# Performance work log

Measured on AMD Instinct MI355X. Metric: run time of the kernel, lower is better.

Reference implementation:

```python
import jax, jax.numpy as jnp
import numpy as np

H_FEATS = 256

def setup_inputs() -> dict:
    key = jax.random.key(0)
    k1, k2, k3, k4, k5, k6, k7 = jax.random.split(key, 7)
    N, E, D = 100000, 500000, H_FEATS
    h = jax.random.normal(k1, (N, D), dtype=jnp.float32)
    src = jax.random.randint(k2, (E,), 0, N)
    dst = jax.random.randint(k3, (E,), 0, N)
    # Linear params (PyTorch default init: U(-1/sqrt(fan_in), 1/sqrt(fan_in)))
    b1_bound = 1.0 / np.sqrt(2 * D)
    b2_bound = 1.0 / np.sqrt(D)
    W1 = jax.random.uniform(k4, (2 * D, D), jnp.float32, -b1_bound, b1_bound)
    b1 = jax.random.uniform(k5, (D,), jnp.float32, -b1_bound, b1_bound)
    W2 = jax.random.uniform(k6, (D, 1), jnp.float32, -b2_bound, b2_bound)
    b2 = jax.random.uniform(k7, (1,), jnp.float32, -b2_bound, b2_bound)
    return {"h": h, "src": src, "dst": dst, "W1": W1, "b1": b1, "W2": W2, "b2": b2}

def reference(h, src, dst, W1, b1, W2, b2):
    # Gather per-edge source/destination node features and concat: [E, 2D]
    he = jnp.concatenate([h[src], h[dst]], axis=1)
    # Linear -> ReLU -> (dropout is identity in eval) -> Linear -> Sigmoid
    hid = jax.nn.relu(he @ W1 + b1)          # [E, D]
    score = jax.nn.sigmoid((hid @ W2 + b2).squeeze(1))  # [E]
    return score
```

## Files before the change

kernel.cpp:

```cpp
#include <hip/hip_runtime.h>
#include <math.h>


typedef __attribute__((ext_vector_type(8))) short short8;
typedef __attribute__((ext_vector_type(2))) float floatx2;
typedef __attribute__((ext_vector_type(4))) float floatx4;
typedef __attribute__((ext_vector_type(16))) float floatx16;

#define D_FEAT 256
#define EPW 8

__device__ __forceinline__ float bf2f(unsigned short u) {
    union { unsigned u32; float f; } v; v.u32 = ((unsigned)u) << 16; return v.f;
}
__device__ __forceinline__ float lo16(unsigned u) {
    union { unsigned u32; float f; } v; v.u32 = u << 16; return v.f;
}
__device__ __forceinline__ float hi16(unsigned u) {
    union { unsigned u32; float f; } v; v.u32 = u & 0xffff0000u; return v.f;
}
__device__ __forceinline__ unsigned short f2bf(float f) {
    union { float f; unsigned u32; } v; v.f = f;
    unsigned x = v.u32;
    return (unsigned short)((x + 0x7fffu + ((x >> 16) & 1u)) >> 16);
}
__device__ __forceinline__ float sigmoid_safe(float r) {
    r = fminf(fmaxf(r, -30.f), 30.f);
    return 1.f / (1.f + expf(-r));
}
__device__ __forceinline__ unsigned pack4_fp8(float a, float b, float c, float d) {
    int w = __builtin_amdgcn_cvt_pk_fp8_f32(a, b, 0, false);
    w = __builtin_amdgcn_cvt_pk_fp8_f32(c, d, w, true);
    return (unsigned)w;
}

__global__ __launch_bounds__(256) void probe_dtype(const unsigned short* __restrict__ h,
                                                   int* __restrict__ flag) {
    __shared__ int cnt[256];
    const int t = threadIdx.x;
    int c = 0;
    #pragma unroll
    for (int i = 0; i < 8; ++i) {
        unsigned e = (h[t * 8 + i] >> 7) & 0xFF;
        c += (e >= 100 && e <= 140) ? 1 : 0;
    }
    cnt[t] = c;
    __syncthreads();
    if (t == 0) {
        int s = 0;
        for (int i = 0; i < 256; ++i) s += cnt[i];
        flag[0] = (s >= 1843) ? 1 : 0;
    }
}

template <int MODE>
__global__ __launch_bounds__(256) void build_wt_t(const void* __restrict__ W1v,
                                                  unsigned short* __restrict__ Wt,
                                                  const int* __restrict__ flag) {
    if (flag[0] != MODE) return;
    int j = blockIdx.x, k = threadIdx.x;
    size_t idx = (j < 256) ? ((size_t)k * 256 + j) : ((size_t)(k + 256) * 256 + (j - 256));
    unsigned short v;
    if constexpr (MODE == 1) v = ((const unsigned short*)W1v)[idx];
    else                     v = f2bf(((const float*)W1v)[idx]);
    Wt[(size_t)j * 256 + k] = v;
}

template <int MODE>
__global__ __launch_bounds__(256, 1) void gemm_pq_t(const void* __restrict__ hv,
                                                    const unsigned short* __restrict__ Wt,
                                                    unsigned char* __restrict__ PQ8,
                                                    int N, const int* __restrict__ flag) {
    if (flag[0] != MODE) return;
    __shared__ unsigned short Bs[256][256];
    __shared__ unsigned short As[64][256];

    const int tid   = threadIdx.x;
    const int lane  = tid & 63;
    const int wid   = tid >> 6;
    const int l32   = lane & 31;
    const int q2    = lane >> 5;
    const int nhalf = blockIdx.x & 1;
    const int mgrp  = blockIdx.x >> 1;
    const int GM    = gridDim.x >> 1;
    const int NT    = (N + 63) >> 6;

    const int hw = tid >> 5;
    const int lb = tid & 31;

    #pragma unroll
    for (int p = 0; p < 4; ++p) {
        short8 v[8];
        #pragma unroll
        for (int i = 0; i < 8; ++i) {
            int r = p * 64 + i * 8 + hw;
            v[i] = *(const short8*)(Wt + (size_t)(nhalf * 256 + r) * 256 + lb * 8);
        }
        #pragma unroll
        for (int i = 0; i < 8; ++i) {
            int r = p * 64 + i * 8 + hw;
            unsigned bo = (unsigned)r * 512 + (((unsigned)lb * 16) ^ (((unsigned)r & 7) << 4));
            *(short8*)((char*)&Bs[0][0] + bo) = v[i];
        }
    }

    short8  pref[8];
    floatx4 pf[16];

    auto load_a = [&](int ms) {
        #pragma unroll
        for (int i = 0; i < 8; ++i) {
            int r = i * 8 + hw;
            int gm = ms * 64 + r;
            if constexpr (MODE == 1) {
                short8 v = {};
                if (gm < N)
                    v = *(const short8*)((const unsigned short*)hv + (size_t)gm * D_FEAT + lb * 8);
                pref[i] = v;
            } else {
                floatx4 f0 = {}, f1 = {};
                if (gm < N) {
                    const float* p = (const float*)hv + (size_t)gm * D_FEAT + lb * 8;
                    f0 = *(const floatx4*)p;
                    f1 = *(const floatx4*)(p + 4);
                }
                pf[2 * i]     = f0;
                pf[2 * i + 1] = f1;
            }
        }
    };

    if (mgrp < NT) load_a(mgrp);

    for (int ms = mgrp; ms < NT; ms += GM) {
        __syncthreads();
        #pragma unroll
        for (int i = 0; i < 8; ++i) {
            int r = i * 8 + hw;
            unsigned bo = (unsigned)r * 512 + (((unsigned)lb * 16) ^ (((unsigned)r & 7) << 4));
            short8 v;
            if constexpr (MODE == 1) {
                v = pref[i];
            } else {
                floatx4 f0 = pf[2 * i], f1 = pf[2 * i + 1];
                v[0] = (short)f2bf(f0.x); v[1] = (short)f2bf(f0.y);
                v[2] = (short)f2bf(f0.z); v[3] = (short)f2bf(f0.w);
                v[4] = (short)f2bf(f1.x); v[5] = (short)f2bf(f1.y);
                v[6] = (short)f2bf(f1.z); v[7] = (short)f2bf(f1.w);
            }
            *(short8*)((char*)&As[0][0] + bo) = v;
        }
        int msn = ms + GM;
        if (msn < NT) load_a(msn);
        __syncthreads();

        floatx16 acc[2][2] = {};
        const int rb0 = wid * 64 + l32;
        #pragma unroll
        for (int ks = 0; ks < 16; ++ks) {
            const unsigned cb = ((unsigned)(ks * 32 + q2 * 16)) ^ (((unsigned)l32 & 7) << 4);
            short8 a0 = *(const short8*)((const char*)&As[0][0] + (unsigned)l32 * 512 + cb);
            short8 a1 = *(const short8*)((const char*)&As[0][0] + (unsigned)(32 + l32) * 512 + cb);
            short8 b0 = *(const short8*)((const char*)&Bs[0][0] + (unsigned)rb0 * 512 + cb);
            short8 b1 = *(const short8*)((const char*)&Bs[0][0] + (unsigned)(rb0 + 32) * 512 + cb);
            acc[0][0] = __builtin_amdgcn_mfma_f32_32x32x16_bf16(b0, a0, acc[0][0], 0, 0, 0);
            acc[0][1] = __builtin_amdgcn_mfma_f32_32x32x16_bf16(b1, a0, acc[0][1], 0, 0, 0);
            acc[1][0] = __builtin_amdgcn_mfma_f32_32x32x16_bf16(b0, a1, acc[1][0], 0, 0, 0);
            acc[1][1] = __builtin_amdgcn_mfma_f32_32x32x16_bf16(b1, a1, acc[1][1], 0, 0, 0);
        }

        const int m_base = ms * 64;
        #pragma unroll
        for (int mi = 0; mi < 2; ++mi) {
            int m = m_base + mi * 32 + l32;
            if (m < N) {
                #pragma unroll
                for (int bj = 0; bj < 2; ++bj) {
                    int nb = nhalf * 256 + wid * 64 + bj * 32 + 4 * q2;
                    #pragma unroll
                    for (int g = 0; g < 4; ++g) {
                        unsigned w = pack4_fp8(acc[mi][bj][4 * g + 0], acc[mi][bj][4 * g + 1],
                                               acc[mi][bj][4 * g + 2], acc[mi][bj][4 * g + 3]);
                        *(unsigned*)(PQ8 + (size_t)m * 512 + nb + 8 * g) = w;
                    }
                }
            }
        }
    }
}

template <int MODE>
__global__ __launch_bounds__(256) void edge_score_t(const unsigned char* __restrict__ PQ8,
                                                    const int* __restrict__ src,
                                                    const int* __restrict__ dst,
                                                    const void* __restrict__ b1v,
                                                    const void* __restrict__ W2v,
                                                    const void* __restrict__ b2v,
                                                    void* __restrict__ outv,
                                                    int E, const int* __restrict__ flag) {
    if (flag[0] != MODE) return;
    const int wave = threadIdx.x >> 6;
    const int lane = threadIdx.x & 63;
    const int e0 = (blockIdx.x * 4 + wave) * EPW;
    if (e0 >= E) return;
    const int l32 = lane & 31;
    const int* __restrict__ idxp = (lane >= 32) ? dst : src;

    float bf[8], wf[8];
    if constexpr (MODE == 1) {
        const uint4 bvr = *(const uint4*)((const unsigned short*)b1v + l32 * 8);
        const uint4 wvr = *(const uint4*)((const unsigned short*)W2v + l32 * 8);
        bf[0] = lo16(bvr.x); bf[1] = hi16(bvr.x); bf[2] = lo16(bvr.y); bf[3] = hi16(bvr.y);
        bf[4] = lo16(bvr.z); bf[5] = hi16(bvr.z); bf[6] = lo16(bvr.w); bf[7] = hi16(bvr.w);
        wf[0] = lo16(wvr.x); wf[1] = hi16(wvr.x); wf[2] = lo16(wvr.y); wf[3] = hi16(wvr.y);
        wf[4] = lo16(wvr.z); wf[5] = hi16(wvr.z); wf[6] = lo16(wvr.w); wf[7] = hi16(wvr.w);
    } else {
        const float* bp = (const float*)b1v + l32 * 8;
        const float* wp = (const float*)W2v + l32 * 8;
        #pragma unroll
        for (int t = 0; t < 8; ++t) { bf[t] = bp[t]; wf[t] = wp[t]; }
    }

    int node[EPW];
    #pragma unroll
    for (int i = 0; i < EPW; ++i) {
        int e = e0 + i; if (e >= E) e = E - 1;
        node[i] = idxp[e];
    }
    uint2 raw[EPW];
    #pragma unroll
    for (int i = 0; i < EPW; ++i)
        raw[i] = *(const uint2*)(PQ8 + (size_t)node[i] * 512 + lane * 8);

    float res[EPW];
    #pragma unroll
    for (int i = 0; i < EPW; ++i) {
        uint2 o;
        o.x = (unsigned)__shfl_xor((int)raw[i].x, 32);
        o.y = (unsigned)__shfl_xor((int)raw[i].y, 32);
        floatx2 p01 = __builtin_amdgcn_cvt_pk_f32_fp8((int)raw[i].x, false);
        floatx2 p23 = __builtin_amdgcn_cvt_pk_f32_fp8((int)raw[i].x, true);
        floatx2 p45 = __builtin_amdgcn_cvt_pk_f32_fp8((int)raw[i].y, false);
        floatx2 p67 = __builtin_amdgcn_cvt_pk_f32_fp8((int)raw[i].y, true);
        floatx2 q01 = __builtin_amdgcn_cvt_pk_f32_fp8((int)o.x, false);
        floatx2 q23 = __builtin_amdgcn_cvt_pk_f32_fp8((int)o.x, true);
        floatx2 q45 = __builtin_amdgcn_cvt_pk_f32_fp8((int)o.y, false);
        floatx2 q67 = __builtin_amdgcn_cvt_pk_f32_fp8((int)o.y, true);
        float v0 = fmaxf(p01.x + q01.x + bf[0], 0.f);
        float v1 = fmaxf(p01.y + q01.y + bf[1], 0.f);
        float v2 = fmaxf(p23.x + q23.x + bf[2], 0.f);
        float v3 = fmaxf(p23.y + q23.y + bf[3], 0.f);
        float v4 = fmaxf(p45.x + q45.x + bf[4], 0.f);
        float v5 = fmaxf(p45.y + q45.y + bf[5], 0.f);
        float v6 = fmaxf(p67.x + q67.x + bf[6], 0.f);
        float v7 = fmaxf(p67.y + q67.y + bf[7], 0.f);
        float sum = v0 * wf[0] + v1 * wf[1] + v2 * wf[2] + v3 * wf[3]
                  + v4 * wf[4] + v5 * wf[5] + v6 * wf[6] + v7 * wf[7];
        #pragma unroll
        for (int off = 1; off <= 16; off <<= 1)
            sum += __shfl_xor(sum, off);
        res[i] = sum;
    }

    if (lane == 0) {
        float bias2;
        if constexpr (MODE == 1) bias2 = bf2f(((const unsigned short*)b2v)[0]);
        else                     bias2 = ((const float*)b2v)[0];
        if constexpr (MODE == 1) {
            union { short8 v; unsigned short u[8]; } r;
            #pragma unroll
            for (int i = 0; i < EPW; ++i)
                r.u[i] = f2bf(sigmoid_safe(res[i] + bias2));
            unsigned short* outp = (unsigned short*)outv;
            if (e0 + EPW <= E) *(short8*)(outp + e0) = r.v;
            else for (int i = 0; i < EPW && e0 + i < E; ++i) outp[e0 + i] = r.u[i];
        } else {
            float* outp = (float*)outv;
            for (int i = 0; i < EPW && e0 + i < E; ++i)
                outp[e0 + i] = sigmoid_safe(res[i] + bias2);
        }
    }
}

template <int MODE>
__global__ __launch_bounds__(256) void edge_fused_t(const void* __restrict__ hv,
                                                    const int* __restrict__ src,
                                                    const int* __restrict__ dst,
                                                    const void* __restrict__ W1v,
                                                    const void* __restrict__ b1v,
                                                    const void* __restrict__ W2v,
                                                    const void* __restrict__ b2v,
                                                    void* __restrict__ outv,
                                                    int E, const int* __restrict__ flag) {
    if (flag && flag[0] != MODE) return;
    __shared__ float he[512];
    __shared__ float wsum[4];
    const int e = blockIdx.x;
    if (e >= E) return;
    const int t = threadIdx.x;
    const int s = src[e];
    const int d = dst[e];

    if constexpr (MODE == 1) {
        he[t]       = bf2f(((const unsigned short*)hv)[(size_t)s * 256 + t]);
        he[256 + t] = bf2f(((const unsigned short*)hv)[(size_t)d * 256 + t]);
    } else {
        he[t]       = ((const float*)hv)[(size_t)s * 256 + t];
        he[256 + t] = ((const float*)hv)[(size_t)d * 256 + t];
    }
    __syncthreads();

    float acc;
    if constexpr (MODE == 1) acc = bf2f(((const unsigned short*)b1v)[t]);
    else                     acc = ((const float*)b1v)[t];

    #pragma unroll 8
    for (int k = 0; k < 512; ++k) {
        float w;
        if constexpr (MODE == 1) w = bf2f(((const unsigned short*)W1v)[(size_t)k * 256 + t]);
        else                     w = ((const float*)W1v)[(size_t)k * 256 + t];
        acc += he[k] * w;
    }

    float w2;
    if constexpr (MODE == 1) w2 = bf2f(((const unsigned short*)W2v)[t]);
    else                     w2 = ((const float*)W2v)[t];
    acc = fmaxf(acc, 0.f) * w2;

    #pragma unroll
    for (int off = 32; off > 0; off >>= 1)
        acc += __shfl_xor(acc, off);
    if ((t & 63) == 0) wsum[t >> 6] = acc;
    __syncthreads();

    if (t == 0) {
        float bias2;
        if constexpr (MODE == 1) bias2 = bf2f(((const unsigned short*)b2v)[0]);
        else                     bias2 = ((const float*)b2v)[0];
        float r = sigmoid_safe(wsum[0] + wsum[1] + wsum[2] + wsum[3] + bias2);
        if constexpr (MODE == 1) ((unsigned short*)outv)[e] = f2bf(r);
        else                     ((float*)outv)[e] = r;
    }
}

extern "C" void kernel_launch(void* const* d_in, const int* in_sizes, int n_in,
                              void* d_out, int out_size, void* d_ws, size_t ws_size,
                              hipStream_t stream) {
    const void* h  = d_in[0];
    const int* src = (const int*)d_in[1];
    const int* dst = (const int*)d_in[2];
    const void* W1 = d_in[3];
    const void* b1 = d_in[4];
    const void* W2 = d_in[5];
    const void* b2 = d_in[6];

    const int N = in_sizes[0] / D_FEAT;
    const int E = in_sizes[1];

    const size_t FLAG_BYTES = 256;
    const size_t wt_bytes  = (size_t)512 * D_FEAT * sizeof(unsigned short);
    const size_t pq_bytes  = (size_t)N * 512;
    const size_t need = FLAG_BYTES + wt_bytes + pq_bytes;

    int* flag = (int*)d_ws;
    unsigned short* Wt = (unsigned short*)((char*)d_ws + FLAG_BYTES);
    unsigned char*  PQ8 = (unsigned char*)((char*)d_ws + FLAG_BYTES + wt_bytes);

    if (ws_size >= need) {
        probe_dtype<<<1, 256, 0, stream>>>((const unsigned short*)h, flag);

        build_wt_t<1><<<512, 256, 0, stream>>>(W1, Wt, flag);
        build_wt_t<0><<<512, 256, 0, stream>>>(W1, Wt, flag);

        gemm_pq_t<1><<<512, 256, 0, stream>>>(h, Wt, PQ8, N, flag);
        gemm_pq_t<0><<<512, 256, 0, stream>>>(h, Wt, PQ8, N, flag);

        int egrid = (E + 4 * EPW - 1) / (4 * EPW);
        edge_score_t<1><<<egrid, 256, 0, stream>>>(PQ8, src, dst, b1, W2, b2, d_out, E, flag);
        edge_score_t<0><<<egrid, 256, 0, stream>>>(PQ8, src, dst, b1, W2, b2, d_out, E, flag);
    } else if (ws_size >= FLAG_BYTES) {
        probe_dtype<<<1, 256, 0, stream>>>((const unsigned short*)h, flag);
        edge_fused_t<1><<<E, 256, 0, stream>>>(h, src, dst, W1, b1, W2, b2, d_out, E, flag);
        edge_fused_t<0><<<E, 256, 0, stream>>>(h, src, dst, W1, b1, W2, b2, d_out, E, flag);
    } else {
        edge_fused_t<1><<<E, 256, 0, stream>>>(h, src, dst, W1, b1, W2, b2, d_out, E, nullptr);
    }
}
```

Measured before the change: 277.1 us.

## Compute full 512-column node projection per block with register-held second half of W

The node GEMM now uses 512-thread blocks that each produce all 512 output columns for a 64-row tile, instead of two blocks splitting the columns. This halves how often each h tile is read and converted. Half of the transposed weight stays in shared memory and the other half is held in registers per wave, with a wider XOR swizzle. The FP8 results are staged through shared memory so each row is written to global memory with coalesced 16-byte stores. The cost is higher register pressure from 16 short8 weight registers per thread, plus two extra barriers per tile.

```diff
diff --git a/kernel.cpp b/kernel.cpp
--- a/kernel.cpp
+++ b/kernel.cpp
@@ -67,7 +67,7 @@
 }
 
 template <int MODE>
-__global__ __launch_bounds__(256, 1) void gemm_pq_t(const void* __restrict__ hv,
+__global__ __launch_bounds__(512, 2) void gemm_pq_t(const void* __restrict__ hv,
                                                     const unsigned short* __restrict__ Wt,
                                                     unsigned char* __restrict__ PQ8,
                                                     int N, const int* __restrict__ flag) {
@@ -75,114 +75,134 @@
     __shared__ unsigned short Bs[256][256];
     __shared__ unsigned short As[64][256];
 
-    const int tid   = threadIdx.x;
-    const int lane  = tid & 63;
-    const int wid   = tid >> 6;
-    const int l32   = lane & 31;
-    const int q2    = lane >> 5;
-    const int nhalf = blockIdx.x & 1;
-    const int mgrp  = blockIdx.x >> 1;
-    const int GM    = gridDim.x >> 1;
-    const int NT    = (N + 63) >> 6;
-
-    const int hw = tid >> 5;
-    const int lb = tid & 31;
-
-    #pragma unroll
-    for (int p = 0; p < 4; ++p) {
-        short8 v[8];
+    const int tid  = threadIdx.x;
+    const int lane = tid & 63;
+    const int wid  = tid >> 6;
+    const int l32  = lane & 31;
+    const int q2   = lane >> 5;
+
+    {
+        const int r = tid >> 1;
+        const unsigned cbase = (tid & 1) * 256;
+        const char* srcp = (const char*)Wt + (size_t)r * 512 + cbase;
+        char* dstb = (char*)&Bs[0][0] + (unsigned)r * 512;
+        const unsigned sw = ((unsigned)r & 31) << 4;
         #pragma unroll
-        for (int i = 0; i < 8; ++i) {
-            int r = p * 64 + i * 8 + hw;
-            v[i] = *(const short8*)(Wt + (size_t)(nhalf * 256 + r) * 256 + lb * 8);
-        }
+        for (int i = 0; i < 16; ++i) {
+            short8 v = *(const short8*)(srcp + i * 16);
+            *(short8*)(dstb + ((cbase + i * 16) ^ sw)) = v;
+        }
+    }
+
+    short8 breg[16];
+    {
+        const char* bp = (const char*)Wt + (size_t)(256 + wid * 32 + l32) * 512 + q2 * 16;
         #pragma unroll
-        for (int i = 0; i < 8; ++i) {
-            int r = p * 64 + i * 8 + hw;
-            unsigned bo = (unsigned)r * 512 + (((unsigned)lb * 16) ^ (((unsigned)r & 7) << 4));
-            *(short8*)((char*)&Bs[0][0] + bo) = v[i];
-        }
-    }
-
-    short8  pref[8];
-    floatx4 pf[16];
-
+        for (int ks = 0; ks < 16; ++ks)
+            breg[ks] = *(const short8*)(bp + ks * 32);
+    }
+
+    const int ar = tid >> 3;
+    const unsigned ac = (unsigned)(tid & 7) * 64;
+    const unsigned aswz = ((unsigned)ar & 31) << 4;
+
+    short8  pref[4];
+    floatx4 pf[8];
     auto load_a = [&](int ms) {
-        #pragma unroll
-        for (int i = 0; i < 8; ++i) {
-            int r = i * 8 + hw;
-            int gm = ms * 64 + r;
-            if constexpr (MODE == 1) {
+        const int gm = ms * 64 + ar;
+        if constexpr (MODE == 1) {
+            #pragma unroll
+            for (int j = 0; j < 4; ++j) {
                 short8 v = {};
                 if (gm < N)
-                    v = *(const short8*)((const unsigned short*)hv + (size_t)gm * D_FEAT + lb * 8);
-                pref[i] = v;
-            } else {
+                    v = *(const short8*)((const char*)hv + (size_t)gm * 512 + ac + j * 16);
+                pref[j] = v;
+            }
+        } else {
+            #pragma unroll
+            for (int j = 0; j < 4; ++j) {
                 floatx4 f0 = {}, f1 = {};
                 if (gm < N) {
-                    const float* p = (const float*)hv + (size_t)gm * D_FEAT + lb * 8;
+                    const float* p = (const float*)hv + (size_t)gm * 256 + (ac + j * 16) / 2;
                     f0 = *(const floatx4*)p;
                     f1 = *(const floatx4*)(p + 4);
                 }
-                pf[2 * i]     = f0;
-                pf[2 * i + 1] = f1;
+                pf[2 * j]     = f0;
+                pf[2 * j + 1] = f1;
             }
         }
     };
 
-    if (mgrp < NT) load_a(mgrp);
-
-    for (int ms = mgrp; ms < NT; ms += GM) {
+    const int NT = (N + 63) >> 6;
+    const int GM = gridDim.x;
+    if ((int)blockIdx.x < NT) load_a(blockIdx.x);
+
+    for (int ms = blockIdx.x; ms < NT; ms += GM) {
         __syncthreads();
-        #pragma unroll
-        for (int i = 0; i < 8; ++i) {
-            int r = i * 8 + hw;
-            unsigned bo = (unsigned)r * 512 + (((unsigned)lb * 16) ^ (((unsigned)r & 7) << 4));
-            short8 v;
-            if constexpr (MODE == 1) {
-                v = pref[i];
-            } else {
-                floatx4 f0 = pf[2 * i], f1 = pf[2 * i + 1];
-                v[0] = (short)f2bf(f0.x); v[1] = (short)f2bf(f0.y);
-                v[2] = (short)f2bf(f0.z); v[3] = (short)f2bf(f0.w);
-                v[4] = (short)f2bf(f1.x); v[5] = (short)f2bf(f1.y);
-                v[6] = (short)f2bf(f1.z); v[7] = (short)f2bf(f1.w);
+        {
+            char* adst = (char*)&As[0][0] + (unsigned)ar * 512;
+            #pragma unroll
+            for (int j = 0; j < 4; ++j) {
+                short8 v;
+                if constexpr (MODE == 1) {
+                    v = pref[j];
+                } else {
+                    floatx4 f0 = pf[2 * j], f1 = pf[2 * j + 1];
+                    v[0] = (short)f2bf(f0.x); v[1] = (short)f2bf(f0.y);
+                    v[2] = (short)f2bf(f0.z); v[3] = (short)f2bf(f0.w);
+                    v[4] = (short)f2bf(f1.x); v[5] = (short)f2bf(f1.y);
+                    v[6] = (short)f2bf(f1.z); v[7] = (short)f2bf(f1.w);
+                }
+                *(short8*)(adst + ((ac + j * 16) ^ aswz)) = v;
             }
-            *(short8*)((char*)&As[0][0] + bo) = v;
-        }
-        int msn = ms + GM;
+        }
+        const int msn = ms + GM;
         if (msn < NT) load_a(msn);
         __syncthreads();
 
         floatx16 acc[2][2] = {};
-        const int rb0 = wid * 64 + l32;
         #pragma unroll
         for (int ks = 0; ks < 16; ++ks) {
-            const unsigned cb = ((unsigned)(ks * 32 + q2 * 16)) ^ (((unsigned)l32 & 7) << 4);
+            const unsigned cb = ((unsigned)(ks * 32 + q2 * 16)) ^ ((unsigned)l32 << 4);
             short8 a0 = *(const short8*)((const char*)&As[0][0] + (unsigned)l32 * 512 + cb);
             short8 a1 = *(const short8*)((const char*)&As[0][0] + (unsigned)(32 + l32) * 512 + cb);
-            short8 b0 = *(const short8*)((const char*)&Bs[0][0] + (unsigned)rb0 * 512 + cb);
-            short8 b1 = *(const short8*)((const char*)&Bs[0][0] + (unsigned)(rb0 + 32) * 512 + cb);
-            acc[0][0] = __builtin_amdgcn_mfma_f32_32x32x16_bf16(b0, a0, acc[0][0], 0, 0, 0);
-            acc[0][1] = __builtin_amdgcn_mfma_f32_32x32x16_bf16(b1, a0, acc[0][1], 0, 0, 0);
-            acc[1][0] = __builtin_amdgcn_mfma_f32_32x32x16_bf16(b0, a1, acc[1][0], 0, 0, 0);
-            acc[1][1] = __builtin_amdgcn_mfma_f32_32x32x16_bf16(b1, a1, acc[1][1], 0, 0, 0);
-        }
-
-        const int m_base = ms * 64;
-        #pragma unroll
-        for (int mi = 0; mi < 2; ++mi) {
-            int m = m_base + mi * 32 + l32;
-            if (m < N) {
+            short8 bl = *(const short8*)((const char*)&Bs[0][0] + (unsigned)(wid * 32 + l32) * 512 + cb);
+            acc[0][0] = __builtin_amdgcn_mfma_f32_32x32x16_bf16(bl,       a0, acc[0][0], 0, 0, 0);
+            acc[1][0] = __builtin_amdgcn_mfma_f32_32x32x16_bf16(bl,       a1, acc[1][0], 0, 0, 0);
+            acc[0][1] = __builtin_amdgcn_mfma_f32_32x32x16_bf16(breg[ks], a0, acc[0][1], 0, 0, 0);
+            acc[1][1] = __builtin_amdgcn_mfma_f32_32x32x16_bf16(breg[ks], a1, acc[1][1], 0, 0, 0);
+        }
+
+        __syncthreads();
+        {
+            unsigned char* scr = (unsigned char*)&As[0][0];
+            #pragma unroll
+            for (int mi = 0; mi < 2; ++mi) {
+                const unsigned row = (unsigned)(mi * 32 + l32);
+                const unsigned rs = (row & 31) << 4;
                 #pragma unroll
-                for (int bj = 0; bj < 2; ++bj) {
-                    int nb = nhalf * 256 + wid * 64 + bj * 32 + 4 * q2;
+                for (int nb = 0; nb < 2; ++nb) {
+                    const unsigned nbase = (unsigned)(nb * 256 + wid * 32 + 4 * q2);
                     #pragma unroll
                     for (int g = 0; g < 4; ++g) {
-                        unsigned w = pack4_fp8(acc[mi][bj][4 * g + 0], acc[mi][bj][4 * g + 1],
-                                               acc[mi][bj][4 * g + 2], acc[mi][bj][4 * g + 3]);
-                        *(unsigned*)(PQ8 + (size_t)m * 512 + nb + 8 * g) = w;
+                        unsigned w = pack4_fp8(acc[mi][nb][4 * g + 0], acc[mi][nb][4 * g + 1],
+                                               acc[mi][nb][4 * g + 2], acc[mi][nb][4 * g + 3]);
+                        const unsigned col = nbase + 8 * g;
+                        *(unsigned*)(scr + ((row * 512 + col) ^ rs)) = w;
                     }
+                }
+            }
+        }
+        __syncthreads();
+        {
+            const unsigned char* scr = (const unsigned char*)&As[0][0];
+            const int gm = ms * 64 + ar;
+            if (gm < N) {
+                #pragma unroll
+                for (int j = 0; j < 4; ++j) {
+                    const unsigned col = ac + j * 16;
+                    uint4 v = *(const uint4*)(scr + (((unsigned)ar * 512 + col) ^ aswz));
+                    *(uint4*)(PQ8 + (size_t)gm * 512 + col) = v;
                 }
             }
         }
@@ -372,8 +392,8 @@
         build_wt_t<1><<<512, 256, 0, stream>>>(W1, Wt, flag);
         build_wt_t<0><<<512, 256, 0, stream>>>(W1, Wt, flag);
 
-        gemm_pq_t<1><<<512, 256, 0, stream>>>(h, Wt, PQ8, N, flag);
-        gemm_pq_t<0><<<512, 256, 0, stream>>>(h, Wt, PQ8, N, flag);
+        gemm_pq_t<1><<<256, 512, 0, stream>>>(h, Wt, PQ8, N, flag);
+        gemm_pq_t<0><<<256, 512, 0, stream>>>(h, Wt, PQ8, N, flag);
 
         int egrid = (E + 4 * EPW - 1) / (4 * EPW);
         edge_score_t<1><<<egrid, 256, 0, stream>>>(PQ8, src, dst, b1, W2, b2, d_out, E, flag);
```

After: 264.7 us. 1.05x faster.
